# Kernel tuning notes

Measured on AMD Instinct MI355X. Metric: run time of the kernel, lower is better.

Reference implementation:

```python
import jax, jax.numpy as jnp
import numpy as np

B, C, H, W = 512, 32, 16, 16
HEADS = 8
D = C * H * W // HEADS  # 1024, per-head flattened dim; Linear is square (D -> D)
W_SCALE = 0.002


def setup_inputs() -> dict:
    key = jax.random.key(0)
    ks = jax.random.split(key, 9)
    f32 = jnp.float32
    return {
        "query": jax.random.normal(ks[0], (B, C, H, W), f32),
        "key": jax.random.normal(ks[1], (B, C, H, W), f32),
        "value": jax.random.normal(ks[2], (B, C, H, W), f32),
        # stacked per-head Linear params: W* is (heads, out=D, in=D) like torch Linear weight
        "W1": jax.random.normal(ks[3], (HEADS, D, D), f32) * W_SCALE,
        "b1": jax.random.normal(ks[4], (HEADS, D), f32) * W_SCALE,
        "W2": jax.random.normal(ks[5], (HEADS, D, D), f32) * W_SCALE,
        "b2": jax.random.normal(ks[6], (HEADS, D), f32) * W_SCALE,
        "W3": jax.random.normal(ks[7], (HEADS, D, D), f32) * W_SCALE,
        "b3": jax.random.normal(ks[8], (HEADS, D), f32) * W_SCALE,
    }


def reference(query, key, value, W1, b1, W2, b2, W3, b3):
    b, c, h, w = query.shape
    heads, d, _ = W1.shape
    # chunk over channels + flatten per head: (b, heads, d)
    q = query.reshape(b, heads, d)
    k = key.reshape(b, heads, d)
    v = value.reshape(b, heads, d)
    # per-head square Linear projections (torch: x @ W.T + b)
    q = jnp.einsum("nhd,hed->nhe", q, W1) + b1
    k = jnp.einsum("nhd,hed->nhe", k, W2) + b2
    v = jnp.einsum("nhd,hed->nhe", v, W3) + b3
    # original divides by p = 1/sqrt(d), i.e. multiplies scores by sqrt(d)
    scale = jnp.sqrt(jnp.asarray(d, q.dtype))
    scores = jnp.einsum("nhe,mhe->hnm", q, k) * scale  # (heads, b, b) attention over batch
    attn = jax.nn.softmax(scores, axis=-1)
    out = jnp.einsum("hnm,mhe->nhe", attn, v)  # (b, heads, d)
    return out.reshape(b, c, h, w)
```

## Files before the change

### kernel.cpp

```cpp
#include <hip/hip_runtime.h>

typedef _Float16 half8 __attribute__((ext_vector_type(8)));
typedef float f32x4 __attribute__((ext_vector_type(4)));

namespace {

constexpr int HEADS = 8;
constexpr int BATCH = 512;
constexpr int DH    = 1024;
constexpr int CHW   = HEADS * DH;

constexpr int BM = 128, BN = 128;

__device__ __forceinline__ int xcd_swz(int bid, int nwg) {
  const int q = nwg >> 3;
  return (bid & 7) * q + (bid >> 3);
}

typedef __attribute__((address_space(3))) unsigned int lds_u32;
typedef const __attribute__((address_space(1))) unsigned int glb_u32;
__device__ __forceinline__ void gl_lds16(const void* g, void* l) {
  __builtin_amdgcn_global_load_lds((glb_u32*)g, (lds_u32*)l, 16, 0, 0);
}

__device__ __forceinline__ half8 cvt8(float4 a, float4 b) {
  half8 r;
  r[0] = (_Float16)a.x; r[1] = (_Float16)a.y; r[2] = (_Float16)a.z; r[3] = (_Float16)a.w;
  r[4] = (_Float16)b.x; r[5] = (_Float16)b.y; r[6] = (_Float16)b.z; r[7] = (_Float16)b.w;
  return r;
}

__global__ __launch_bounds__(256) void proj_kernel(
    const float* __restrict__ Xq, const float* __restrict__ Xk, const float* __restrict__ Xv,
    const float* __restrict__ W1, const float* __restrict__ b1,
    const float* __restrict__ W2, const float* __restrict__ b2,
    const float* __restrict__ W3, const float* __restrict__ b3,
    _Float16* __restrict__ Qp, _Float16* __restrict__ Kp, _Float16* __restrict__ VpT) {
  __shared__ __align__(16) float As[BM * 32];
  __shared__ __align__(16) float Bs[BN * 32];
  const int tid = threadIdx.x;
  const int l  = xcd_swz(blockIdx.x, 768);
  const int z  = l >> 8, rem = l & 255;
  const int h  = rem >> 5, bx = rem & 31;
  const int tm = bx & 3, tn = bx >> 2;
  const float* X    = (z == 0) ? Xq : (z == 1) ? Xk : Xv;
  const float* W    = (z == 0) ? W1 : (z == 1) ? W2 : W3;
  const float* bias = (z == 0) ? b1 : (z == 1) ? b2 : b3;
  _Float16*    P    = (z == 0) ? Qp : (z == 1) ? Kp : VpT;

  const int lane = tid & 63, w = tid >> 6;
  const int wr = (w >> 1) * 64, wc = (w & 1) * 64;
  const int lr = lane & 15, lk = lane >> 4;

  const char* Ab = (const char*)(X + (size_t)tm * BM * CHW + (size_t)h * DH);
  const char* Bb = (const char*)(W + (size_t)h * DH * DH + (size_t)tn * BN * DH);

  const char* srcA0; const char* srcA1; const char* srcA2; const char* srcA3;
  const char* srcB0; const char* srcB1; const char* srcB2; const char* srcB3;
  int off0, off1, off2, off3;
  {
    int off, row, scb;
    off = 0 * 4096 + tid * 16; row = off >> 7; scb = ((off >> 4) & 7) ^ (row & 7);
    off0 = off; srcA0 = Ab + (size_t)row * (CHW * 4) + scb * 16; srcB0 = Bb + (size_t)row * (DH * 4) + scb * 16;
    off = 1 * 4096 + tid * 16; row = off >> 7; scb = ((off >> 4) & 7) ^ (row & 7);
    off1 = off; srcA1 = Ab + (size_t)row * (CHW * 4) + scb * 16; srcB1 = Bb + (size_t)row * (DH * 4) + scb * 16;
    off = 2 * 4096 + tid * 16; row = off >> 7; scb = ((off >> 4) & 7) ^ (row & 7);
    off2 = off; srcA2 = Ab + (size_t)row * (CHW * 4) + scb * 16; srcB2 = Bb + (size_t)row * (DH * 4) + scb * 16;
    off = 3 * 4096 + tid * 16; row = off >> 7; scb = ((off >> 4) & 7) ^ (row & 7);
    off3 = off; srcA3 = Ab + (size_t)row * (CHW * 4) + scb * 16; srcB3 = Bb + (size_t)row * (DH * 4) + scb * 16;
  }

  constexpr int NT = DH / 32;
  f32x4 acc[4][4] = {};
#pragma unroll 1
  for (int t = 0; t < NT; ++t) {
    __syncthreads();
    gl_lds16(srcA0, (char*)As + off0); gl_lds16(srcB0, (char*)Bs + off0);
    gl_lds16(srcA1, (char*)As + off1); gl_lds16(srcB1, (char*)Bs + off1);
    gl_lds16(srcA2, (char*)As + off2); gl_lds16(srcB2, (char*)Bs + off2);
    gl_lds16(srcA3, (char*)As + off3); gl_lds16(srcB3, (char*)Bs + off3);
    srcA0 += 128; srcA1 += 128; srcA2 += 128; srcA3 += 128;
    srcB0 += 128; srcB1 += 128; srcB2 += 128; srcB3 += 128;
    __syncthreads();
    half8 av[4], bv[4];
#pragma unroll
    for (int i = 0; i < 4; ++i) {
      const int row = wr + i * 16 + lr;
      const float4 p0 = *(const float4*)&As[row * 32 + (((lk * 2)    ) ^ (row & 7)) * 4];
      const float4 p1 = *(const float4*)&As[row * 32 + (((lk * 2 + 1)) ^ (row & 7)) * 4];
      av[i] = cvt8(p0, p1);
    }
#pragma unroll
    for (int j = 0; j < 4; ++j) {
      const int row = wc + j * 16 + lr;
      const float4 p0 = *(const float4*)&Bs[row * 32 + (((lk * 2)    ) ^ (row & 7)) * 4];
      const float4 p1 = *(const float4*)&Bs[row * 32 + (((lk * 2 + 1)) ^ (row & 7)) * 4];
      bv[j] = cvt8(p0, p1);
    }
#pragma unroll
    for (int i = 0; i < 4; ++i)
#pragma unroll
      for (int j = 0; j < 4; ++j)
        acc[i][j] = __builtin_amdgcn_mfma_f32_16x16x32_f16(av[i], bv[j], acc[i][j], 0, 0, 0);
  }

#pragma unroll
  for (int i = 0; i < 4; ++i)
#pragma unroll
    for (int j = 0; j < 4; ++j) {
      const int e = tn * BN + wc + j * 16 + lr;
      const float bb = bias[h * DH + e];
#pragma unroll
      for (int q = 0; q < 4; ++q) {
        const int n = tm * BM + wr + i * 16 + lk * 4 + q;
        const float val = acc[i][j][q] + bb;
        if (z != 2) P[((size_t)h * BATCH + n) * DH + e] = (_Float16)val;
        else        P[((size_t)h * DH + e) * BATCH + n] = (_Float16)val;
      }
    }
}

template <int NT>
__device__ __forceinline__ void gemm16_core(
    const char* ga, size_t lda, const char* gb, size_t ldb,
    _Float16* As, _Float16* Bs,
    int tid, int wr, int wc, int lr, int lk, f32x4 (&acc)[4][4]) {
  const char* srcA0; const char* srcA1; const char* srcA2; const char* srcA3;
  const char* srcB0; const char* srcB1; const char* srcB2; const char* srcB3;
  int off0, off1, off2, off3;
  {
    int off, row, scb;
    off = 0 * 4096 + tid * 16; row = off >> 7; scb = ((off >> 4) & 7) ^ (row & 7);
    off0 = off; srcA0 = ga + (size_t)row * lda + scb * 16; srcB0 = gb + (size_t)row * ldb + scb * 16;
    off = 1 * 4096 + tid * 16; row = off >> 7; scb = ((off >> 4) & 7) ^ (row & 7);
    off1 = off; srcA1 = ga + (size_t)row * lda + scb * 16; srcB1 = gb + (size_t)row * ldb + scb * 16;
    off = 2 * 4096 + tid * 16; row = off >> 7; scb = ((off >> 4) & 7) ^ (row & 7);
    off2 = off; srcA2 = ga + (size_t)row * lda + scb * 16; srcB2 = gb + (size_t)row * ldb + scb * 16;
    off = 3 * 4096 + tid * 16; row = off >> 7; scb = ((off >> 4) & 7) ^ (row & 7);
    off3 = off; srcA3 = ga + (size_t)row * lda + scb * 16; srcB3 = gb + (size_t)row * ldb + scb * 16;
  }

#pragma unroll 1
  for (int t = 0; t < NT; ++t) {
    __syncthreads();
    gl_lds16(srcA0, (char*)As + off0); gl_lds16(srcB0, (char*)Bs + off0);
    gl_lds16(srcA1, (char*)As + off1); gl_lds16(srcB1, (char*)Bs + off1);
    gl_lds16(srcA2, (char*)As + off2); gl_lds16(srcB2, (char*)Bs + off2);
    gl_lds16(srcA3, (char*)As + off3); gl_lds16(srcB3, (char*)Bs + off3);
    srcA0 += 128; srcA1 += 128; srcA2 += 128; srcA3 += 128;
    srcB0 += 128; srcB1 += 128; srcB2 += 128; srcB3 += 128;
    __syncthreads();
    half8 a0[4], a1[4], b0[4], b1[4];
#pragma unroll
    for (int i = 0; i < 4; ++i) {
      const int row = wr + i * 16 + lr;
      a0[i] = *(const half8*)&As[row * 64 + ((lk    ) ^ (row & 7)) * 8];
      a1[i] = *(const half8*)&As[row * 64 + ((4 + lk) ^ (row & 7)) * 8];
    }
#pragma unroll
    for (int j = 0; j < 4; ++j) {
      const int row = wc + j * 16 + lr;
      b0[j] = *(const half8*)&Bs[row * 64 + ((lk    ) ^ (row & 7)) * 8];
      b1[j] = *(const half8*)&Bs[row * 64 + ((4 + lk) ^ (row & 7)) * 8];
    }
#pragma unroll
    for (int i = 0; i < 4; ++i)
#pragma unroll
      for (int j = 0; j < 4; ++j) {
        acc[i][j] = __builtin_amdgcn_mfma_f32_16x16x32_f16(a0[i], b0[j], acc[i][j], 0, 0, 0);
        acc[i][j] = __builtin_amdgcn_mfma_f32_16x16x32_f16(a1[i], b1[j], acc[i][j], 0, 0, 0);
      }
  }
}

__global__ __launch_bounds__(256) void score_kernel(
    const _Float16* __restrict__ Qp, const _Float16* __restrict__ Kp,
    float* __restrict__ S) {
  __shared__ __align__(16) _Float16 As[BM * 64];
  __shared__ __align__(16) _Float16 Bs[BN * 64];
  const int tid = threadIdx.x;
  const int l  = xcd_swz(blockIdx.x, 128);
  const int h  = l >> 4, bx = l & 15;
  const int tm = bx & 3, tn = bx >> 2;
  const int lane = tid & 63, w = tid >> 6;
  const int wr = (w >> 1) * 64, wc = (w & 1) * 64;
  const int lr = lane & 15, lk = lane >> 4;

  const char* ga = (const char*)(Qp + ((size_t)h * BATCH + tm * BM) * DH);
  const char* gb = (const char*)(Kp + ((size_t)h * BATCH + tn * BN) * DH);

  f32x4 acc[4][4] = {};
  gemm16_core<DH / 64>(ga, DH * 2, gb, DH * 2, As, Bs, tid, wr, wc, lr, lk, acc);

#pragma unroll
  for (int i = 0; i < 4; ++i)
#pragma unroll
    for (int j = 0; j < 4; ++j) {
      const int m = tn * BN + wc + j * 16 + lr;
#pragma unroll
      for (int q = 0; q < 4; ++q) {
        const int n = tm * BM + wr + i * 16 + lk * 4 + q;
        S[((size_t)h * BATCH + n) * BATCH + m] = 32.0f * acc[i][j][q];
      }
    }
}

__global__ __launch_bounds__(64) void softmax_kernel(
    const float* __restrict__ S, _Float16* __restrict__ A) {
  const size_t r = (size_t)blockIdx.x * BATCH;
  const int l = threadIdx.x;
  float v[8];
  float mx = -1e30f;
#pragma unroll
  for (int i = 0; i < 8; ++i) { v[i] = S[r + i * 64 + l]; mx = fmaxf(mx, v[i]); }
#pragma unroll
  for (int off = 32; off; off >>= 1) mx = fmaxf(mx, __shfl_xor(mx, off));
  float sum = 0.f;
#pragma unroll
  for (int i = 0; i < 8; ++i) { v[i] = __expf(v[i] - mx); sum += v[i]; }
#pragma unroll
  for (int off = 32; off; off >>= 1) sum += __shfl_xor(sum, off);
  const float inv = 1.f / sum;
#pragma unroll
  for (int i = 0; i < 8; ++i) A[r + i * 64 + l] = (_Float16)(v[i] * inv);
}

__global__ __launch_bounds__(256) void pv_kernel(
    const _Float16* __restrict__ At, const _Float16* __restrict__ VpT,
    float* __restrict__ Out) {
  __shared__ __align__(16) _Float16 As[BM * 64];
  __shared__ __align__(16) _Float16 Bs[BN * 64];
  const int tid = threadIdx.x;
  const int l  = xcd_swz(blockIdx.x, 256);
  const int h  = l >> 5, bx = l & 31;
  const int tm = bx & 3, tn = bx >> 2;
  const int lane = tid & 63, w = tid >> 6;
  const int wr = (w >> 1) * 64, wc = (w & 1) * 64;
  const int lr = lane & 15, lk = lane >> 4;

  const char* ga = (const char*)(At  + ((size_t)h * BATCH + tm * BM) * BATCH);
  const char* gb = (const char*)(VpT + ((size_t)h * DH   + tn * BN) * BATCH);

  f32x4 acc[4][4] = {};
  gemm16_core<BATCH / 64>(ga, BATCH * 2, gb, BATCH * 2, As, Bs, tid, wr, wc, lr, lk, acc);

#pragma unroll
  for (int i = 0; i < 4; ++i)
#pragma unroll
    for (int j = 0; j < 4; ++j) {
      const int e = tn * BN + wc + j * 16 + lr;
#pragma unroll
      for (int q = 0; q < 4; ++q) {
        const int n = tm * BM + wr + i * 16 + lk * 4 + q;
        Out[((size_t)n * HEADS + h) * DH + e] = acc[i][j][q];
      }
    }
}

}

extern "C" void kernel_launch(void* const* d_in, const int* in_sizes, int n_in,
                              void* d_out, int out_size, void* d_ws, size_t ws_size,
                              hipStream_t stream) {
  (void)in_sizes; (void)n_in; (void)out_size; (void)ws_size;
  const float* q  = (const float*)d_in[0];
  const float* k  = (const float*)d_in[1];
  const float* v  = (const float*)d_in[2];
  const float* W1 = (const float*)d_in[3];
  const float* b1 = (const float*)d_in[4];
  const float* W2 = (const float*)d_in[5];
  const float* b2 = (const float*)d_in[6];
  const float* W3 = (const float*)d_in[7];
  const float* b3 = (const float*)d_in[8];
  float* out = (float*)d_out;

  _Float16* Qp  = (_Float16*)d_ws;
  _Float16* Kp  = Qp + (size_t)BATCH * HEADS * DH;
  _Float16* VpT = Kp + (size_t)BATCH * HEADS * DH;
  float*    S   = (float*)(VpT + (size_t)BATCH * HEADS * DH);
  _Float16* At  = (_Float16*)(S + (size_t)HEADS * BATCH * BATCH);

  const dim3 blk(256);
  proj_kernel<<<dim3(768), blk, 0, stream>>>(q, k, v, W1, b1, W2, b2, W3, b3, Qp, Kp, VpT);
  score_kernel<<<dim3(128), blk, 0, stream>>>(Qp, Kp, S);
  softmax_kernel<<<dim3(HEADS * BATCH), dim3(64), 0, stream>>>(S, At);
  pv_kernel<<<dim3(256), blk, 0, stream>>>(At, VpT, out);
}
```

Measured before the change: 108.5 us.

## Restructure projection GEMM with 256x256 tiles, register-prefetch and fp16 LDS staging

The projection kernel moves from 128x128 tiles with 256 threads to 256x256 tiles with 512 threads. Global loads now go into registers two K-steps ahead, are converted to fp16 once, and are written into double-buffered padded fp16 LDS, so the fp32 global-to-LDS direct loads and the repeated per-wave conversions go away. This aims to raise data reuse and overlap loads with MFMA work. In exchange the accumulators double, which raises register pressure, and the grid shrinks to 192 blocks, which may leave CUs underused on a 256-CU device.

```diff
diff --git a/kernel.cpp b/kernel.cpp
--- a/kernel.cpp
+++ b/kernel.cpp
@@ -9,8 +9,6 @@
 constexpr int BATCH = 512;
 constexpr int DH    = 1024;
 constexpr int CHW   = HEADS * DH;
-
-constexpr int BM = 128, BN = 128;
 
 __device__ __forceinline__ int xcd_swz(int bid, int nwg) {
   const int q = nwg >> 3;
@@ -30,95 +28,131 @@
   return r;
 }
 
-__global__ __launch_bounds__(256) void proj_kernel(
+constexpr int PLDW = 40;
+
+__device__ __forceinline__ void stage_write(
+    _Float16* Ad, _Float16* Bd, int so,
+    float4 a0, float4 a1, float4 a2, float4 a3,
+    float4 b0, float4 b1, float4 b2, float4 b3) {
+  *(half8*)&Ad[so]     = cvt8(a0, a1);
+  *(half8*)&Ad[so + 8] = cvt8(a2, a3);
+  *(half8*)&Bd[so]     = cvt8(b0, b1);
+  *(half8*)&Bd[so + 8] = cvt8(b2, b3);
+}
+
+__global__ __launch_bounds__(512) void proj_kernel(
     const float* __restrict__ Xq, const float* __restrict__ Xk, const float* __restrict__ Xv,
     const float* __restrict__ W1, const float* __restrict__ b1,
     const float* __restrict__ W2, const float* __restrict__ b2,
     const float* __restrict__ W3, const float* __restrict__ b3,
     _Float16* __restrict__ Qp, _Float16* __restrict__ Kp, _Float16* __restrict__ VpT) {
-  __shared__ __align__(16) float As[BM * 32];
-  __shared__ __align__(16) float Bs[BN * 32];
+  __shared__ __align__(16) _Float16 As[2][256 * PLDW];
+  __shared__ __align__(16) _Float16 Bs[2][256 * PLDW];
   const int tid = threadIdx.x;
-  const int l  = xcd_swz(blockIdx.x, 768);
-  const int z  = l >> 8, rem = l & 255;
-  const int h  = rem >> 5, bx = rem & 31;
-  const int tm = bx & 3, tn = bx >> 2;
+  const int l  = xcd_swz(blockIdx.x, 192);
+  const int g  = l >> 3, bx = l & 7;
+  const int z  = g >> 3, h = g & 7;
+  const int tm = bx >> 2, tn = bx & 3;
   const float* X    = (z == 0) ? Xq : (z == 1) ? Xk : Xv;
   const float* W    = (z == 0) ? W1 : (z == 1) ? W2 : W3;
   const float* bias = (z == 0) ? b1 : (z == 1) ? b2 : b3;
   _Float16*    P    = (z == 0) ? Qp : (z == 1) ? Kp : VpT;
 
   const int lane = tid & 63, w = tid >> 6;
-  const int wr = (w >> 1) * 64, wc = (w & 1) * 64;
+  const int wr2 = (w >> 2) * 128, wc2 = (w & 3) * 64;
   const int lr = lane & 15, lk = lane >> 4;
-
-  const char* Ab = (const char*)(X + (size_t)tm * BM * CHW + (size_t)h * DH);
-  const char* Bb = (const char*)(W + (size_t)h * DH * DH + (size_t)tn * BN * DH);
-
-  const char* srcA0; const char* srcA1; const char* srcA2; const char* srcA3;
-  const char* srcB0; const char* srcB1; const char* srcB2; const char* srcB3;
-  int off0, off1, off2, off3;
-  {
-    int off, row, scb;
-    off = 0 * 4096 + tid * 16; row = off >> 7; scb = ((off >> 4) & 7) ^ (row & 7);
-    off0 = off; srcA0 = Ab + (size_t)row * (CHW * 4) + scb * 16; srcB0 = Bb + (size_t)row * (DH * 4) + scb * 16;
-    off = 1 * 4096 + tid * 16; row = off >> 7; scb = ((off >> 4) & 7) ^ (row & 7);
-    off1 = off; srcA1 = Ab + (size_t)row * (CHW * 4) + scb * 16; srcB1 = Bb + (size_t)row * (DH * 4) + scb * 16;
-    off = 2 * 4096 + tid * 16; row = off >> 7; scb = ((off >> 4) & 7) ^ (row & 7);
-    off2 = off; srcA2 = Ab + (size_t)row * (CHW * 4) + scb * 16; srcB2 = Bb + (size_t)row * (DH * 4) + scb * 16;
-    off = 3 * 4096 + tid * 16; row = off >> 7; scb = ((off >> 4) & 7) ^ (row & 7);
-    off3 = off; srcA3 = Ab + (size_t)row * (CHW * 4) + scb * 16; srcB3 = Bb + (size_t)row * (DH * 4) + scb * 16;
+  const int srow = tid >> 1, sc0 = (tid & 1) * 16;
+  const int so = srow * PLDW + sc0;
+
+  const float* ga = X + (size_t)(tm * 256 + srow) * CHW + (size_t)h * DH + sc0;
+  const float* gb = W + (size_t)h * DH * DH + (size_t)(tn * 256 + srow) * DH + sc0;
+
+  constexpr int NT = DH / 32;
+  float4 pa0, pa1, pa2, pa3, pb0, pb1, pb2, pb3;
+  float4 qa0, qa1, qa2, qa3, qb0, qb1, qb2, qb3;
+
+  pa0 = ((const float4*)ga)[0]; pa1 = ((const float4*)ga)[1];
+  pa2 = ((const float4*)ga)[2]; pa3 = ((const float4*)ga)[3];
+  pb0 = ((const float4*)gb)[0]; pb1 = ((const float4*)gb)[1];
+  pb2 = ((const float4*)gb)[2]; pb3 = ((const float4*)gb)[3];
+  ga += 32; gb += 32;
+  qa0 = ((const float4*)ga)[0]; qa1 = ((const float4*)ga)[1];
+  qa2 = ((const float4*)ga)[2]; qa3 = ((const float4*)ga)[3];
+  qb0 = ((const float4*)gb)[0]; qb1 = ((const float4*)gb)[1];
+  qb2 = ((const float4*)gb)[2]; qb3 = ((const float4*)gb)[3];
+  ga += 32; gb += 32;
+  stage_write(As[0], Bs[0], so, pa0, pa1, pa2, pa3, pb0, pb1, pb2, pb3);
+  __syncthreads();
+
+  f32x4 acc[8][4] = {};
+#pragma unroll 1
+  for (int t = 0; t < NT; t += 2) {
+    if (t + 2 < NT) {
+      pa0 = ((const float4*)ga)[0]; pa1 = ((const float4*)ga)[1];
+      pa2 = ((const float4*)ga)[2]; pa3 = ((const float4*)ga)[3];
+      pb0 = ((const float4*)gb)[0]; pb1 = ((const float4*)gb)[1];
+      pb2 = ((const float4*)gb)[2]; pb3 = ((const float4*)gb)[3];
+      ga += 32; gb += 32;
+    }
+    {
+      half8 av[8], bv[4];
+#pragma unroll
+      for (int i = 0; i < 8; ++i)
+        av[i] = *(const half8*)&As[0][(wr2 + i * 16 + lr) * PLDW + lk * 8];
+#pragma unroll
+      for (int j = 0; j < 4; ++j)
+        bv[j] = *(const half8*)&Bs[0][(wc2 + j * 16 + lr) * PLDW + lk * 8];
+#pragma unroll
+      for (int i = 0; i < 8; ++i)
+#pragma unroll
+        for (int j = 0; j < 4; ++j)
+          acc[i][j] = __builtin_amdgcn_mfma_f32_16x16x32_f16(av[i], bv[j], acc[i][j], 0, 0, 0);
+    }
+    stage_write(As[1], Bs[1], so, qa0, qa1, qa2, qa3, qb0, qb1, qb2, qb3);
+    __syncthreads();
+    if (t + 3 < NT) {
+      qa0 = ((const float4*)ga)[0]; qa1 = ((const float4*)ga)[1];
+      qa2 = ((const float4*)ga)[2]; qa3 = ((const float4*)ga)[3];
+      qb0 = ((const float4*)gb)[0]; qb1 = ((const float4*)gb)[1];
+      qb2 = ((const float4*)gb)[2]; qb3 = ((const float4*)gb)[3];
+      ga += 32; gb += 32;
+    }
+    {
+      half8 av[8], bv[4];
+#pragma unroll
+      for (int i = 0; i < 8; ++i)
+        av[i] = *(const half8*)&As[1][(wr2 + i * 16 + lr) * PLDW + lk * 8];
+#pragma unroll
+      for (int j = 0; j < 4; ++j)
+        bv[j] = *(const half8*)&Bs[1][(wc2 + j * 16 + lr) * PLDW + lk * 8];
+#pragma unroll
+      for (int i = 0; i < 8; ++i)
+#pragma unroll
+        for (int j = 0; j < 4; ++j)
+          acc[i][j] = __builtin_amdgcn_mfma_f32_16x16x32_f16(av[i], bv[j], acc[i][j], 0, 0, 0);
+    }
+    if (t + 2 < NT)
+      stage_write(As[0], Bs[0], so, pa0, pa1, pa2, pa3, pb0, pb1, pb2, pb3);
+    __syncthreads();
   }
 
-  constexpr int NT = DH / 32;
-  f32x4 acc[4][4] = {};
-#pragma unroll 1
-  for (int t = 0; t < NT; ++t) {
-    __syncthreads();
-    gl_lds16(srcA0, (char*)As + off0); gl_lds16(srcB0, (char*)Bs + off0);
-    gl_lds16(srcA1, (char*)As + off1); gl_lds16(srcB1, (char*)Bs + off1);
-    gl_lds16(srcA2, (char*)As + off2); gl_lds16(srcB2, (char*)Bs + off2);
-    gl_lds16(srcA3, (char*)As + off3); gl_lds16(srcB3, (char*)Bs + off3);
-    srcA0 += 128; srcA1 += 128; srcA2 += 128; srcA3 += 128;
-    srcB0 += 128; srcB1 += 128; srcB2 += 128; srcB3 += 128;
-    __syncthreads();
-    half8 av[4], bv[4];
-#pragma unroll
-    for (int i = 0; i < 4; ++i) {
-      const int row = wr + i * 16 + lr;
-      const float4 p0 = *(const float4*)&As[row * 32 + (((lk * 2)    ) ^ (row & 7)) * 4];
-      const float4 p1 = *(const float4*)&As[row * 32 + (((lk * 2 + 1)) ^ (row & 7)) * 4];
-      av[i] = cvt8(p0, p1);
-    }
+#pragma unroll
+  for (int i = 0; i < 8; ++i)
 #pragma unroll
     for (int j = 0; j < 4; ++j) {
-      const int row = wc + j * 16 + lr;
-      const float4 p0 = *(const float4*)&Bs[row * 32 + (((lk * 2)    ) ^ (row & 7)) * 4];
-      const float4 p1 = *(const float4*)&Bs[row * 32 + (((lk * 2 + 1)) ^ (row & 7)) * 4];
-      bv[j] = cvt8(p0, p1);
-    }
-#pragma unroll
-    for (int i = 0; i < 4; ++i)
-#pragma unroll
-      for (int j = 0; j < 4; ++j)
-        acc[i][j] = __builtin_amdgcn_mfma_f32_16x16x32_f16(av[i], bv[j], acc[i][j], 0, 0, 0);
-  }
-
-#pragma unroll
-  for (int i = 0; i < 4; ++i)
-#pragma unroll
-    for (int j = 0; j < 4; ++j) {
-      const int e = tn * BN + wc + j * 16 + lr;
+      const int e = tn * 256 + wc2 + j * 16 + lr;
       const float bb = bias[h * DH + e];
 #pragma unroll
       for (int q = 0; q < 4; ++q) {
-        const int n = tm * BM + wr + i * 16 + lk * 4 + q;
+        const int n = tm * 256 + wr2 + i * 16 + lk * 4 + q;
         const float val = acc[i][j][q] + bb;
         if (z != 2) P[((size_t)h * BATCH + n) * DH + e] = (_Float16)val;
         else        P[((size_t)h * DH + e) * BATCH + n] = (_Float16)val;
       }
     }
 }
+
+constexpr int BM = 128, BN = 128;
 
 template <int NT>
 __device__ __forceinline__ void gemm16_core(
@@ -280,9 +314,8 @@
   float*    S   = (float*)(VpT + (size_t)BATCH * HEADS * DH);
   _Float16* At  = (_Float16*)(S + (size_t)HEADS * BATCH * BATCH);
 
-  const dim3 blk(256);
-  proj_kernel<<<dim3(768), blk, 0, stream>>>(q, k, v, W1, b1, W2, b2, W3, b3, Qp, Kp, VpT);
-  score_kernel<<<dim3(128), blk, 0, stream>>>(Qp, Kp, S);
+  proj_kernel<<<dim3(192), dim3(512), 0, stream>>>(q, k, v, W1, b1, W2, b2, W3, b3, Qp, Kp, VpT);
+  score_kernel<<<dim3(128), dim3(256), 0, stream>>>(Qp, Kp, S);
   softmax_kernel<<<dim3(HEADS * BATCH), dim3(64), 0, stream>>>(S, At);
-  pv_kernel<<<dim3(256), blk, 0, stream>>>(At, VpT, out);
-}
+  pv_kernel<<<dim3(256), dim3(256), 0, stream>>>(At, VpT, out);
+}
```

Result: slower. 115.1 us (+6.0%).

## Pre-pack inputs and weights into swizzled fp16 tiles for contiguous GEMM loads

Applied to the files above, without the earlier changes.

Adds a pack kernel that converts X and W from fp32 to fp16 and lays them out in tile-contiguous, XOR-swizzled 128x64 blocks. All GEMM kernels, and the producer epilogues of proj and softmax, now use this packed layout, so each k-step copies contiguous 16 KB chunks into LDS. The projection now reads half the bytes per k-step and skips the in-loop fp32-to-fp16 conversion. In exchange it adds an extra launch and a full fp32 read plus fp16 write of 24M weight elements on every call, and the scattered epilogue stores are less coalesced. Workspace buffers are aliased to reuse memory.

```diff
diff --git a/kernel.cpp b/kernel.cpp
--- a/kernel.cpp
+++ b/kernel.cpp
@@ -1,6 +1,7 @@
 #include <hip/hip_runtime.h>
 
 typedef _Float16 half8 __attribute__((ext_vector_type(8)));
+typedef _Float16 half4 __attribute__((ext_vector_type(4)));
 typedef float f32x4 __attribute__((ext_vector_type(4)));
 
 namespace {
@@ -8,9 +9,7 @@
 constexpr int HEADS = 8;
 constexpr int BATCH = 512;
 constexpr int DH    = 1024;
-constexpr int CHW   = HEADS * DH;
-
-constexpr int BM = 128, BN = 128;
+constexpr int CHW   = 8192;
 
 __device__ __forceinline__ int xcd_swz(int bid, int nwg) {
   const int q = nwg >> 3;
@@ -23,152 +22,149 @@
   __builtin_amdgcn_global_load_lds((glb_u32*)g, (lds_u32*)l, 16, 0, 0);
 }
 
-__device__ __forceinline__ half8 cvt8(float4 a, float4 b) {
-  half8 r;
+__device__ __forceinline__ half4 cvt4(float4 a) {
+  half4 r;
   r[0] = (_Float16)a.x; r[1] = (_Float16)a.y; r[2] = (_Float16)a.z; r[3] = (_Float16)a.w;
-  r[4] = (_Float16)b.x; r[5] = (_Float16)b.y; r[6] = (_Float16)b.z; r[7] = (_Float16)b.w;
   return r;
 }
 
+__global__ __launch_bounds__(256) void pack_kernel(
+    const float* __restrict__ Xq, const float* __restrict__ Xk, const float* __restrict__ Xv,
+    const float* __restrict__ W1, const float* __restrict__ W2, const float* __restrict__ W3,
+    _Float16* __restrict__ Xp, _Float16* __restrict__ Wp) {
+  const int l = xcd_swz(blockIdx.x, 288);
+  const int t = threadIdx.x;
+  const int kt = t >> 4;
+  const int cbn = (t & 15) >> 1;
+  const int hi  = (t & 1) * 4;
+  const float* src;
+  size_t srcStride;
+  _Float16* dstBase;
+  if (l < 192) {
+    const int z = l >> 6, rem = l & 63, h = rem >> 3, et = rem & 7;
+    const float* W = (z == 0) ? W1 : (z == 1) ? W2 : W3;
+    src = W + (size_t)h * DH * DH + (size_t)et * 128 * DH + t * 4;
+    srcStride = DH;
+    dstBase = Wp + ((((size_t)z * 8 + h) * 8 + et) * 16 + kt) * 8192;
+  } else {
+    const int l2 = l - 192;
+    const int z = l2 >> 5, rem = l2 & 31, h = rem >> 2, nt = rem & 3;
+    const float* X = (z == 0) ? Xq : (z == 1) ? Xk : Xv;
+    src = X + (size_t)nt * 128 * CHW + (size_t)h * DH + t * 4;
+    srcStride = CHW;
+    dstBase = Xp + ((((size_t)z * 8 + h) * 4 + nt) * 16 + kt) * 8192;
+  }
+#pragma unroll 1
+  for (int r = 0; r < 128; r += 4) {
+    float4 v0 = *(const float4*)(src + (size_t)(r + 0) * srcStride);
+    float4 v1 = *(const float4*)(src + (size_t)(r + 1) * srcStride);
+    float4 v2 = *(const float4*)(src + (size_t)(r + 2) * srcStride);
+    float4 v3 = *(const float4*)(src + (size_t)(r + 3) * srcStride);
+    *(half4*)&dstBase[(r + 0) * 64 + (cbn ^ ((r + 0) & 7)) * 8 + hi] = cvt4(v0);
+    *(half4*)&dstBase[(r + 1) * 64 + (cbn ^ ((r + 1) & 7)) * 8 + hi] = cvt4(v1);
+    *(half4*)&dstBase[(r + 2) * 64 + (cbn ^ ((r + 2) & 7)) * 8 + hi] = cvt4(v2);
+    *(half4*)&dstBase[(r + 3) * 64 + (cbn ^ ((r + 3) & 7)) * 8 + hi] = cvt4(v3);
+  }
+}
+
+template <int NT>
+__device__ __forceinline__ void gemm16p_core(
+    const char* ga, const char* gb,
+    _Float16* As, _Float16* Bs,
+    int tid, int wr, int wc, int lr, int lk, f32x4 (&acc)[4][4]) {
+  const int off0 = tid * 16, off1 = 4096 + tid * 16;
+  const int off2 = 8192 + tid * 16, off3 = 12288 + tid * 16;
+#pragma unroll 1
+  for (int t = 0; t < NT; ++t) {
+    __syncthreads();
+    gl_lds16(ga + off0, (char*)As + off0); gl_lds16(gb + off0, (char*)Bs + off0);
+    gl_lds16(ga + off1, (char*)As + off1); gl_lds16(gb + off1, (char*)Bs + off1);
+    gl_lds16(ga + off2, (char*)As + off2); gl_lds16(gb + off2, (char*)Bs + off2);
+    gl_lds16(ga + off3, (char*)As + off3); gl_lds16(gb + off3, (char*)Bs + off3);
+    ga += 16384; gb += 16384;
+    __syncthreads();
+    half8 a0[4], a1[4], b0[4], b1[4];
+#pragma unroll
+    for (int i = 0; i < 4; ++i) {
+      const int row = wr + i * 16 + lr;
+      a0[i] = *(const half8*)&As[row * 64 + ((lk    ) ^ (row & 7)) * 8];
+      a1[i] = *(const half8*)&As[row * 64 + ((4 + lk) ^ (row & 7)) * 8];
+    }
+#pragma unroll
+    for (int j = 0; j < 4; ++j) {
+      const int row = wc + j * 16 + lr;
+      b0[j] = *(const half8*)&Bs[row * 64 + ((lk    ) ^ (row & 7)) * 8];
+      b1[j] = *(const half8*)&Bs[row * 64 + ((4 + lk) ^ (row & 7)) * 8];
+    }
+#pragma unroll
+    for (int i = 0; i < 4; ++i)
+#pragma unroll
+      for (int j = 0; j < 4; ++j) {
+        acc[i][j] = __builtin_amdgcn_mfma_f32_16x16x32_f16(a0[i], b0[j], acc[i][j], 0, 0, 0);
+        acc[i][j] = __builtin_amdgcn_mfma_f32_16x16x32_f16(a1[i], b1[j], acc[i][j], 0, 0, 0);
+      }
+  }
+}
+
 __global__ __launch_bounds__(256) void proj_kernel(
-    const float* __restrict__ Xq, const float* __restrict__ Xk, const float* __restrict__ Xv,
-    const float* __restrict__ W1, const float* __restrict__ b1,
-    const float* __restrict__ W2, const float* __restrict__ b2,
-    const float* __restrict__ W3, const float* __restrict__ b3,
-    _Float16* __restrict__ Qp, _Float16* __restrict__ Kp, _Float16* __restrict__ VpT) {
-  __shared__ __align__(16) float As[BM * 32];
-  __shared__ __align__(16) float Bs[BN * 32];
+    const _Float16* __restrict__ Xp, const _Float16* __restrict__ Wp,
+    const float* __restrict__ b1, const float* __restrict__ b2, const float* __restrict__ b3,
+    _Float16* __restrict__ Qp, _Float16* __restrict__ Kp, _Float16* __restrict__ Vp) {
+  __shared__ __align__(16) _Float16 As[128 * 64];
+  __shared__ __align__(16) _Float16 Bs[128 * 64];
   const int tid = threadIdx.x;
   const int l  = xcd_swz(blockIdx.x, 768);
   const int z  = l >> 8, rem = l & 255;
   const int h  = rem >> 5, bx = rem & 31;
   const int tm = bx & 3, tn = bx >> 2;
-  const float* X    = (z == 0) ? Xq : (z == 1) ? Xk : Xv;
-  const float* W    = (z == 0) ? W1 : (z == 1) ? W2 : W3;
   const float* bias = (z == 0) ? b1 : (z == 1) ? b2 : b3;
-  _Float16*    P    = (z == 0) ? Qp : (z == 1) ? Kp : VpT;
 
   const int lane = tid & 63, w = tid >> 6;
   const int wr = (w >> 1) * 64, wc = (w & 1) * 64;
   const int lr = lane & 15, lk = lane >> 4;
 
-  const char* Ab = (const char*)(X + (size_t)tm * BM * CHW + (size_t)h * DH);
-  const char* Bb = (const char*)(W + (size_t)h * DH * DH + (size_t)tn * BN * DH);
-
-  const char* srcA0; const char* srcA1; const char* srcA2; const char* srcA3;
-  const char* srcB0; const char* srcB1; const char* srcB2; const char* srcB3;
-  int off0, off1, off2, off3;
-  {
-    int off, row, scb;
-    off = 0 * 4096 + tid * 16; row = off >> 7; scb = ((off >> 4) & 7) ^ (row & 7);
-    off0 = off; srcA0 = Ab + (size_t)row * (CHW * 4) + scb * 16; srcB0 = Bb + (size_t)row * (DH * 4) + scb * 16;
-    off = 1 * 4096 + tid * 16; row = off >> 7; scb = ((off >> 4) & 7) ^ (row & 7);
-    off1 = off; srcA1 = Ab + (size_t)row * (CHW * 4) + scb * 16; srcB1 = Bb + (size_t)row * (DH * 4) + scb * 16;
-    off = 2 * 4096 + tid * 16; row = off >> 7; scb = ((off >> 4) & 7) ^ (row & 7);
-    off2 = off; srcA2 = Ab + (size_t)row * (CHW * 4) + scb * 16; srcB2 = Bb + (size_t)row * (DH * 4) + scb * 16;
-    off = 3 * 4096 + tid * 16; row = off >> 7; scb = ((off >> 4) & 7) ^ (row & 7);
-    off3 = off; srcA3 = Ab + (size_t)row * (CHW * 4) + scb * 16; srcB3 = Bb + (size_t)row * (DH * 4) + scb * 16;
-  }
-
-  constexpr int NT = DH / 32;
+  const char* ga = (const char*)(Xp + ((((size_t)z * 8 + h) * 4 + tm) * 16) * 8192);
+  const char* gb = (const char*)(Wp + ((((size_t)z * 8 + h) * 8 + tn) * 16) * 8192);
+
   f32x4 acc[4][4] = {};
-#pragma unroll 1
-  for (int t = 0; t < NT; ++t) {
-    __syncthreads();
-    gl_lds16(srcA0, (char*)As + off0); gl_lds16(srcB0, (char*)Bs + off0);
-    gl_lds16(srcA1, (char*)As + off1); gl_lds16(srcB1, (char*)Bs + off1);
-    gl_lds16(srcA2, (char*)As + off2); gl_lds16(srcB2, (char*)Bs + off2);
-    gl_lds16(srcA3, (char*)As + off3); gl_lds16(srcB3, (char*)Bs + off3);
-    srcA0 += 128; srcA1 += 128; srcA2 += 128; srcA3 += 128;
-    srcB0 += 128; srcB1 += 128; srcB2 += 128; srcB3 += 128;
-    __syncthreads();
-    half8 av[4], bv[4];
-#pragma unroll
-    for (int i = 0; i < 4; ++i) {
-      const int row = wr + i * 16 + lr;
-      const float4 p0 = *(const float4*)&As[row * 32 + (((lk * 2)    ) ^ (row & 7)) * 4];
-      const float4 p1 = *(const float4*)&As[row * 32 + (((lk * 2 + 1)) ^ (row & 7)) * 4];
-      av[i] = cvt8(p0, p1);
-    }
-#pragma unroll
-    for (int j = 0; j < 4; ++j) {
-      const int row = wc + j * 16 + lr;
-      const float4 p0 = *(const float4*)&Bs[row * 32 + (((lk * 2)    ) ^ (row & 7)) * 4];
-      const float4 p1 = *(const float4*)&Bs[row * 32 + (((lk * 2 + 1)) ^ (row & 7)) * 4];
-      bv[j] = cvt8(p0, p1);
-    }
+  gemm16p_core<16>(ga, gb, As, Bs, tid, wr, wc, lr, lk, acc);
+
+  if (z != 2) {
+    _Float16* P = (z == 0) ? Qp : Kp;
 #pragma unroll
     for (int i = 0; i < 4; ++i)
 #pragma unroll
-      for (int j = 0; j < 4; ++j)
-        acc[i][j] = __builtin_amdgcn_mfma_f32_16x16x32_f16(av[i], bv[j], acc[i][j], 0, 0, 0);
-  }
-
-#pragma unroll
-  for (int i = 0; i < 4; ++i)
-#pragma unroll
-    for (int j = 0; j < 4; ++j) {
-      const int e = tn * BN + wc + j * 16 + lr;
-      const float bb = bias[h * DH + e];
-#pragma unroll
-      for (int q = 0; q < 4; ++q) {
-        const int n = tm * BM + wr + i * 16 + lk * 4 + q;
-        const float val = acc[i][j][q] + bb;
-        if (z != 2) P[((size_t)h * BATCH + n) * DH + e] = (_Float16)val;
-        else        P[((size_t)h * DH + e) * BATCH + n] = (_Float16)val;
-      }
-    }
-}
-
-template <int NT>
-__device__ __forceinline__ void gemm16_core(
-    const char* ga, size_t lda, const char* gb, size_t ldb,
-    _Float16* As, _Float16* Bs,
-    int tid, int wr, int wc, int lr, int lk, f32x4 (&acc)[4][4]) {
-  const char* srcA0; const char* srcA1; const char* srcA2; const char* srcA3;
-  const char* srcB0; const char* srcB1; const char* srcB2; const char* srcB3;
-  int off0, off1, off2, off3;
-  {
-    int off, row, scb;
-    off = 0 * 4096 + tid * 16; row = off >> 7; scb = ((off >> 4) & 7) ^ (row & 7);
-    off0 = off; srcA0 = ga + (size_t)row * lda + scb * 16; srcB0 = gb + (size_t)row * ldb + scb * 16;
-    off = 1 * 4096 + tid * 16; row = off >> 7; scb = ((off >> 4) & 7) ^ (row & 7);
-    off1 = off; srcA1 = ga + (size_t)row * lda + scb * 16; srcB1 = gb + (size_t)row * ldb + scb * 16;
-    off = 2 * 4096 + tid * 16; row = off >> 7; scb = ((off >> 4) & 7) ^ (row & 7);
-    off2 = off; srcA2 = ga + (size_t)row * lda + scb * 16; srcB2 = gb + (size_t)row * ldb + scb * 16;
-    off = 3 * 4096 + tid * 16; row = off >> 7; scb = ((off >> 4) & 7) ^ (row & 7);
-    off3 = off; srcA3 = ga + (size_t)row * lda + scb * 16; srcB3 = gb + (size_t)row * ldb + scb * 16;
-  }
-
-#pragma unroll 1
-  for (int t = 0; t < NT; ++t) {
-    __syncthreads();
-    gl_lds16(srcA0, (char*)As + off0); gl_lds16(srcB0, (char*)Bs + off0);
-    gl_lds16(srcA1, (char*)As + off1); gl_lds16(srcB1, (char*)Bs + off1);
-    gl_lds16(srcA2, (char*)As + off2); gl_lds16(srcB2, (char*)Bs + off2);
-    gl_lds16(srcA3, (char*)As + off3); gl_lds16(srcB3, (char*)Bs + off3);
-    srcA0 += 128; srcA1 += 128; srcA2 += 128; srcA3 += 128;
-    srcB0 += 128; srcB1 += 128; srcB2 += 128; srcB3 += 128;
-    __syncthreads();
-    half8 a0[4], a1[4], b0[4], b1[4];
-#pragma unroll
-    for (int i = 0; i < 4; ++i) {
-      const int row = wr + i * 16 + lr;
-      a0[i] = *(const half8*)&As[row * 64 + ((lk    ) ^ (row & 7)) * 8];
-      a1[i] = *(const half8*)&As[row * 64 + ((4 + lk) ^ (row & 7)) * 8];
-    }
-#pragma unroll
-    for (int j = 0; j < 4; ++j) {
-      const int row = wc + j * 16 + lr;
-      b0[j] = *(const half8*)&Bs[row * 64 + ((lk    ) ^ (row & 7)) * 8];
-      b1[j] = *(const half8*)&Bs[row * 64 + ((4 + lk) ^ (row & 7)) * 8];
-    }
+      for (int j = 0; j < 4; ++j) {
+        const int colj = wc + j * 16 + lr;
+        const int e = tn * 128 + colj;
+        const float bb = bias[h * DH + e];
+        const int kte = tn * 2 + (colj >> 6);
+        const int c64 = colj & 63;
+        const int cbn = c64 >> 3;
+#pragma unroll
+        for (int q = 0; q < 4; ++q) {
+          const int row = wr + i * 16 + lk * 4 + q;
+          const float val = acc[i][j][q] + bb;
+          P[(((size_t)h * 4 + tm) * 16 + kte) * 8192 +
+            row * 64 + ((cbn ^ (row & 7)) * 8) + (c64 & 7)] = (_Float16)val;
+        }
+      }
+  } else {
 #pragma unroll
     for (int i = 0; i < 4; ++i)
 #pragma unroll
       for (int j = 0; j < 4; ++j) {
-        acc[i][j] = __builtin_amdgcn_mfma_f32_16x16x32_f16(a0[i], b0[j], acc[i][j], 0, 0, 0);
-        acc[i][j] = __builtin_amdgcn_mfma_f32_16x16x32_f16(a1[i], b1[j], acc[i][j], 0, 0, 0);
+        const int row_v = wc + j * 16 + lr;
+        const float bb = bias[h * DH + tn * 128 + row_v];
+#pragma unroll
+        for (int q = 0; q < 4; ++q) {
+          const int n = tm * 128 + wr + i * 16 + lk * 4 + q;
+          const float val = acc[i][j][q] + bb;
+          const int c64 = n & 63;
+          const int cbn = c64 >> 3;
+          Vp[(((size_t)h * 8 + tn) * 8 + (n >> 6)) * 8192 +
+             row_v * 64 + ((cbn ^ (row_v & 7)) * 8) + (n & 7)] = (_Float16)val;
+        }
       }
   }
 }
@@ -176,8 +172,8 @@
 __global__ __launch_bounds__(256) void score_kernel(
     const _Float16* __restrict__ Qp, const _Float16* __restrict__ Kp,
     float* __restrict__ S) {
-  __shared__ __align__(16) _Float16 As[BM * 64];
-  __shared__ __align__(16) _Float16 Bs[BN * 64];
+  __shared__ __align__(16) _Float16 As[128 * 64];
+  __shared__ __align__(16) _Float16 Bs[128 * 64];
   const int tid = threadIdx.x;
   const int l  = xcd_swz(blockIdx.x, 128);
   const int h  = l >> 4, bx = l & 15;
@@ -186,27 +182,28 @@
   const int wr = (w >> 1) * 64, wc = (w & 1) * 64;
   const int lr = lane & 15, lk = lane >> 4;
 
-  const char* ga = (const char*)(Qp + ((size_t)h * BATCH + tm * BM) * DH);
-  const char* gb = (const char*)(Kp + ((size_t)h * BATCH + tn * BN) * DH);
+  const char* ga = (const char*)(Qp + (((size_t)h * 4 + tm) * 16) * 8192);
+  const char* gb = (const char*)(Kp + (((size_t)h * 4 + tn) * 16) * 8192);
 
   f32x4 acc[4][4] = {};
-  gemm16_core<DH / 64>(ga, DH * 2, gb, DH * 2, As, Bs, tid, wr, wc, lr, lk, acc);
+  gemm16p_core<16>(ga, gb, As, Bs, tid, wr, wc, lr, lk, acc);
 
 #pragma unroll
   for (int i = 0; i < 4; ++i)
 #pragma unroll
     for (int j = 0; j < 4; ++j) {
-      const int m = tn * BN + wc + j * 16 + lr;
+      const int m = tn * 128 + wc + j * 16 + lr;
 #pragma unroll
       for (int q = 0; q < 4; ++q) {
-        const int n = tm * BM + wr + i * 16 + lk * 4 + q;
+        const int n = tm * 128 + wr + i * 16 + lk * 4 + q;
         S[((size_t)h * BATCH + n) * BATCH + m] = 32.0f * acc[i][j][q];
       }
     }
 }
 
 __global__ __launch_bounds__(64) void softmax_kernel(
-    const float* __restrict__ S, _Float16* __restrict__ A) {
+    const float* __restrict__ S, _Float16* __restrict__ Ap) {
+  const int h = blockIdx.x >> 9, n = blockIdx.x & 511;
   const size_t r = (size_t)blockIdx.x * BATCH;
   const int l = threadIdx.x;
   float v[8];
@@ -221,15 +218,19 @@
 #pragma unroll
   for (int off = 32; off; off >>= 1) sum += __shfl_xor(sum, off);
   const float inv = 1.f / sum;
-#pragma unroll
-  for (int i = 0; i < 8; ++i) A[r + i * 64 + l] = (_Float16)(v[i] * inv);
+  const int row = n & 127;
+  const int cbs = ((l >> 3) ^ (row & 7)) * 8 + (l & 7);
+  const size_t base = (((size_t)h * 4 + (n >> 7)) * 8) * 8192 + row * 64 + cbs;
+#pragma unroll
+  for (int i = 0; i < 8; ++i)
+    Ap[base + (size_t)i * 8192] = (_Float16)(v[i] * inv);
 }
 
 __global__ __launch_bounds__(256) void pv_kernel(
-    const _Float16* __restrict__ At, const _Float16* __restrict__ VpT,
+    const _Float16* __restrict__ Ap, const _Float16* __restrict__ Vp,
     float* __restrict__ Out) {
-  __shared__ __align__(16) _Float16 As[BM * 64];
-  __shared__ __align__(16) _Float16 Bs[BN * 64];
+  __shared__ __align__(16) _Float16 As[128 * 64];
+  __shared__ __align__(16) _Float16 Bs[128 * 64];
   const int tid = threadIdx.x;
   const int l  = xcd_swz(blockIdx.x, 256);
   const int h  = l >> 5, bx = l & 31;
@@ -238,20 +239,20 @@
   const int wr = (w >> 1) * 64, wc = (w & 1) * 64;
   const int lr = lane & 15, lk = lane >> 4;
 
-  const char* ga = (const char*)(At  + ((size_t)h * BATCH + tm * BM) * BATCH);
-  const char* gb = (const char*)(VpT + ((size_t)h * DH   + tn * BN) * BATCH);
+  const char* ga = (const char*)(Ap + (((size_t)h * 4 + tm) * 8) * 8192);
+  const char* gb = (const char*)(Vp + (((size_t)h * 8 + tn) * 8) * 8192);
 
   f32x4 acc[4][4] = {};
-  gemm16_core<BATCH / 64>(ga, BATCH * 2, gb, BATCH * 2, As, Bs, tid, wr, wc, lr, lk, acc);
+  gemm16p_core<8>(ga, gb, As, Bs, tid, wr, wc, lr, lk, acc);
 
 #pragma unroll
   for (int i = 0; i < 4; ++i)
 #pragma unroll
     for (int j = 0; j < 4; ++j) {
-      const int e = tn * BN + wc + j * 16 + lr;
+      const int e = tn * 128 + wc + j * 16 + lr;
 #pragma unroll
       for (int q = 0; q < 4; ++q) {
-        const int n = tm * BM + wr + i * 16 + lk * 4 + q;
+        const int n = tm * 128 + wr + i * 16 + lk * 4 + q;
         Out[((size_t)n * HEADS + h) * DH + e] = acc[i][j][q];
       }
     }
@@ -274,15 +275,17 @@
   const float* b3 = (const float*)d_in[8];
   float* out = (float*)d_out;
 
-  _Float16* Qp  = (_Float16*)d_ws;
-  _Float16* Kp  = Qp + (size_t)BATCH * HEADS * DH;
-  _Float16* VpT = Kp + (size_t)BATCH * HEADS * DH;
-  float*    S   = (float*)(VpT + (size_t)BATCH * HEADS * DH);
-  _Float16* At  = (_Float16*)(S + (size_t)HEADS * BATCH * BATCH);
-
-  const dim3 blk(256);
-  proj_kernel<<<dim3(768), blk, 0, stream>>>(q, k, v, W1, b1, W2, b2, W3, b3, Qp, Kp, VpT);
-  score_kernel<<<dim3(128), blk, 0, stream>>>(Qp, Kp, S);
-  softmax_kernel<<<dim3(HEADS * BATCH), dim3(64), 0, stream>>>(S, At);
-  pv_kernel<<<dim3(256), blk, 0, stream>>>(At, VpT, out);
-}
+  _Float16* Xp = (_Float16*)d_ws;
+  _Float16* Wp = Xp + (size_t)12582912;
+  _Float16* Qp = Wp + (size_t)25165824;
+  _Float16* Kp = Qp + (size_t)4194304;
+  _Float16* Vp = Kp + (size_t)4194304;
+  float*    S  = (float*)Xp;
+  _Float16* Ap = Wp;
+
+  pack_kernel<<<dim3(288), dim3(256), 0, stream>>>(q, k, v, W1, W2, W3, Xp, Wp);
+  proj_kernel<<<dim3(768), dim3(256), 0, stream>>>(Xp, Wp, b1, b2, b3, Qp, Kp, Vp);
+  score_kernel<<<dim3(128), dim3(256), 0, stream>>>(Qp, Kp, S);
+  softmax_kernel<<<dim3(HEADS * BATCH), dim3(64), 0, stream>>>(S, Ap);
+  pv_kernel<<<dim3(256), dim3(256), 0, stream>>>(Ap, Vp, out);
+}
```

Result: slower. 120.4 us (+10.9%).
